# Kernel optimization log

Hardware: AMD Instinct MI355X
Metric: run time of the kernel (lower is better)

## Reference

```python
import jax, jax.numpy as jnp
import numpy as np

EMBED_DIM = 1024
NUM_HEADS = 16
ROTARY_THETA = 10000.0


def _rotate_half(t):
    d = t.shape[-1] // 2
    t1, t2 = t[..., :d], t[..., d:]
    return jnp.concatenate([-t2, t1], axis=-1)


def _rope_cos_sin(seq_len, head_dim, dtype):
    # inv_freq over even indices, standard RoPE
    inv_freq = 1.0 / (ROTARY_THETA ** (jnp.arange(0, head_dim, 2, dtype=jnp.float32) / head_dim))
    freqs = jnp.arange(seq_len, dtype=jnp.float32)[:, None] * inv_freq[None, :]  # (S, D/2)
    emb = jnp.concatenate([freqs, freqs], axis=-1)  # (S, D)
    # broadcast over (b, s, h, d)
    return jnp.cos(emb).astype(dtype)[None, :, None, :], jnp.sin(emb).astype(dtype)[None, :, None, :]


def setup_inputs() -> dict:
    key = jax.random.key(0)
    ks = jax.random.split(key, 4)
    B, S, E = 2, 2048, EMBED_DIM
    scale = 1.0 / np.sqrt(E)
    return {
        "x": jax.random.normal(ks[0], (B, S, E), dtype=jnp.float32),
        "attention_mask": jnp.zeros((B, 1, 1, S), dtype=jnp.float32),
        "Wq": jax.random.normal(ks[1], (E, E), dtype=jnp.float32) * scale,
        "bq": jnp.zeros((E,), dtype=jnp.float32),
        "Wk": jax.random.normal(ks[2], (E, E), dtype=jnp.float32) * scale,
        "bk": jnp.zeros((E,), dtype=jnp.float32),
        "Wv": jax.random.normal(ks[3], (E, E), dtype=jnp.float32) * scale,
        "bv": jnp.zeros((E,), dtype=jnp.float32),
    }


def reference(x, attention_mask, Wq, bq, Wk, bk, Wv, bv):
    B, S, E = x.shape
    H = NUM_HEADS
    D = E // H

    q = (x @ Wq + bq).reshape(B, S, H, D)
    k = (x @ Wk + bk).reshape(B, S, H, D)
    v = (x @ Wv + bv).reshape(B, S, H, D)

    cos, sin = _rope_cos_sin(S, D, q.dtype)
    q = q * cos + _rotate_half(q) * sin
    k = k * cos + _rotate_half(k) * sin

    # attention_mask: additive padding bias (b,1,1,k) broadcast over heads & queries
    scores = jnp.einsum("bqhd,bkhd->bhqk", q, k) / jnp.sqrt(jnp.asarray(D, dtype=q.dtype))
    scores = scores + attention_mask  # broadcasts to (b,h,q,k)
    attn = jax.nn.softmax(scores, axis=-1)
    out = jnp.einsum("bhqk,bkhd->bqhd", attn, v)
    return out.reshape(B, S, E)
```

## Files before the change

### kernel.cpp

```cpp
#include <hip/hip_runtime.h>

typedef __attribute__((ext_vector_type(8)))  short bf16x8;
typedef __attribute__((ext_vector_type(4)))  float f32x4;
typedef __attribute__((ext_vector_type(16))) float f32x16;
typedef __attribute__((ext_vector_type(4)))  unsigned u32x4;
typedef __attribute__((ext_vector_type(4)))  _Float16 f16x4;

#define B_  2
#define S_  2048
#define H_  16
#define D_  64
#define E_  1024
#define M_  (B_*S_)
#define L2E 1.44269504f

__device__ __forceinline__ unsigned short f2bf(float f){
  unsigned x = __builtin_bit_cast(unsigned, f);
  x += 0x7fffu + ((x >> 16) & 1u);
  return (unsigned short)(x >> 16);
}
__device__ __forceinline__ unsigned pk_bf16(float lo, float hi){
  unsigned short a = __builtin_bit_cast(unsigned short, (__bf16)lo);
  unsigned short b = __builtin_bit_cast(unsigned short, (__bf16)hi);
  return (unsigned)a | ((unsigned)b << 16);
}

#define GLD16(gp, lp) __builtin_amdgcn_global_load_lds( \
    (const __attribute__((address_space(1))) unsigned*)(gp), \
    (__attribute__((address_space(3))) unsigned*)(lp), 16, 0, 0)

__global__ __launch_bounds__(256) void k_tables(const float* __restrict__ mask,
                                                float* ct, float* st, float* maskC){
  int i = blockIdx.x*256 + threadIdx.x;
  int s = i >> 5, f = i & 31;
  float invf = powf(10000.0f, -(float)f / 32.0f);
  float ph = (float)s * invf;
  ct[i] = cosf(ph);
  st[i] = sinf(ph);
  if(i < B_*S_) maskC[i] = fmaf(mask[i], L2E, -17.0f);
}

__global__ __launch_bounds__(256) void k_cvt(const float* __restrict__ in, short* __restrict__ out){
  int i = (blockIdx.x*256 + threadIdx.x)*4;
  float4 v = *(const float4*)(in + i);
  typedef __attribute__((ext_vector_type(4))) short s16x4;
  s16x4 o = { (short)f2bf(v.x), (short)f2bf(v.y), (short)f2bf(v.z), (short)f2bf(v.w) };
  *(s16x4*)(out + i) = o;
}

__global__ __launch_bounds__(256) void k_wt(const float* __restrict__ Wq, const float* __restrict__ Wk,
                                            const float* __restrict__ Wv, short* __restrict__ wt){
  const float* W = blockIdx.z==0 ? Wq : (blockIdx.z==1 ? Wk : Wv);
  short* out = wt + (size_t)blockIdx.z*E_*E_;
  __shared__ short tile[64][72];
  int nb = blockIdx.x*64, kb = blockIdx.y*64;
  int t = threadIdx.x;
  {
    int r = t>>2, c0 = (t&3)*16;
    const float* src = W + (size_t)(kb+r)*E_ + nb + c0;
    #pragma unroll
    for(int i=0;i<4;i++){
      float4 v = *(const float4*)(src + i*4);
      tile[r][c0+i*4+0] = (short)f2bf(v.x);
      tile[r][c0+i*4+1] = (short)f2bf(v.y);
      tile[r][c0+i*4+2] = (short)f2bf(v.z);
      tile[r][c0+i*4+3] = (short)f2bf(v.w);
    }
  }
  __syncthreads();
  {
    int n = t>>2, k0 = (t&3)*16;
    short* dst = out + (size_t)(nb+n)*E_ + kb + k0;
    bf16x8 o0, o1;
    #pragma unroll
    for(int i=0;i<8;i++){ o0[i] = tile[k0+i][n]; o1[i] = tile[k0+8+i][n]; }
    *(bf16x8*)dst = o0;
    *(bf16x8*)(dst+8) = o1;
  }
}

__global__ __launch_bounds__(256) void k_gemm(const short* __restrict__ A, const short* __restrict__ WT,
                                              const float* __restrict__ biasq, const float* __restrict__ biask,
                                              const float* __restrict__ biasv,
                                              short* __restrict__ oq, short* __restrict__ ok, short* __restrict__ ov,
                                              const float* __restrict__ cost, const float* __restrict__ sint){
  const int z = blockIdx.z;
  const short* Bw = WT + (size_t)z*E_*E_;
  const float* bias = z==0 ? biasq : (z==1 ? biask : biasv);
  short* out = z==0 ? oq : (z==1 ? ok : ov);
  __shared__ short As[128*32];
  __shared__ short Bs[128*32];
  const int t = threadIdx.x, lane = t & 63, wid = t >> 6;
  const int mb = blockIdx.x*128, nb = blockIdx.y*128;
  const int wm = (wid>>1)*64, wn = (wid&1)*64;
  f32x4 acc[4][4] = {};
  for(int kt=0; kt<E_/32; kt++){
    __syncthreads();
    {
      int f0 = t, f1 = t + 256;
      GLD16(A  + (size_t)(mb + (f0>>2))*E_ + kt*32 + (f0&3)*8, &As[f0*8]);
      GLD16(A  + (size_t)(mb + (f1>>2))*E_ + kt*32 + (f1&3)*8, &As[f1*8]);
      GLD16(Bw + (size_t)(nb + (f0>>2))*E_ + kt*32 + (f0&3)*8, &Bs[f0*8]);
      GLD16(Bw + (size_t)(nb + (f1>>2))*E_ + kt*32 + (f1&3)*8, &Bs[f1*8]);
    }
    __syncthreads();
    bf16x8 af[4], bfv[4];
    #pragma unroll
    for(int mf=0; mf<4; mf++)
      af[mf] = *(const bf16x8*)&As[(wm + mf*16 + (lane&15))*32 + (lane>>4)*8];
    #pragma unroll
    for(int nf=0; nf<4; nf++)
      bfv[nf] = *(const bf16x8*)&Bs[(wn + nf*16 + (lane&15))*32 + (lane>>4)*8];
    #pragma unroll
    for(int mf=0; mf<4; mf++)
      #pragma unroll
      for(int nf=0; nf<4; nf++)
        acc[mf][nf] = __builtin_amdgcn_mfma_f32_16x16x32_bf16(af[mf], bfv[nf], acc[mf][nf], 0, 0, 0);
  }
  const int col16 = lane & 15, rg = lane >> 4;
  float bvs[4];
  #pragma unroll
  for(int nf=0; nf<4; nf++) bvs[nf] = bias[nb + wn + nf*16 + col16];
  if(z == 2){
    #pragma unroll
    for(int mf=0; mf<4; mf++)
      #pragma unroll
      for(int nf=0; nf<4; nf++)
        #pragma unroll
        for(int r=0; r<4; r++){
          int row = mb + wm + mf*16 + rg*4 + r;
          out[(size_t)row*E_ + nb + wn + nf*16 + col16] = (short)f2bf(acc[mf][nf][r] + bvs[nf]);
        }
  } else {
    const float qs = (z==0) ? (0.125f*L2E) : 1.0f;
    #pragma unroll
    for(int mf=0; mf<4; mf++)
      #pragma unroll
      for(int r=0; r<4; r++){
        int row = mb + wm + mf*16 + rg*4 + r;
        int srow = row & (S_-1);
        const float* cb = cost + (size_t)srow*32;
        const float* sb = sint + (size_t)srow*32;
        #pragma unroll
        for(int nf=0; nf<2; nf++){
          int d = nf*16 + col16;
          float c = cb[d], sn = sb[d];
          float x0 = acc[mf][nf][r]   + bvs[nf];
          float x1 = acc[mf][nf+2][r] + bvs[nf+2];
          out[(size_t)row*E_ + nb + wn + nf*16 + col16]     = (short)f2bf((x0*c - x1*sn)*qs);
          out[(size_t)row*E_ + nb + wn + (nf+2)*16 + col16] = (short)f2bf((x1*c + x0*sn)*qs);
        }
      }
  }
}

__global__ __launch_bounds__(256) void k_vt(const short* __restrict__ v, short* __restrict__ vt){
  __shared__ short tl[64][72];
  const int b = blockIdx.z, h = blockIdx.y, s0 = blockIdx.x*64;
  const int t = threadIdx.x;
  {
    int r = t>>2, c0 = (t&3)*16;
    const short* src = v + ((size_t)(b*S_ + s0 + r)*H_ + h)*D_ + c0;
    *(bf16x8*)&tl[r][c0]   = *(const bf16x8*)src;
    *(bf16x8*)&tl[r][c0+8] = *(const bf16x8*)(src+8);
  }
  __syncthreads();
  {
    int d = t>>2, t0 = (t&3)*16;
    short* dst = vt + ((size_t)(b*H_ + h)*D_ + d)*S_ + s0 + t0;
    bf16x8 o0, o1;
    #pragma unroll
    for(int i=0;i<8;i++){ o0[i] = tl[t0+i][d]; o1[i] = tl[t0+8+i][d]; }
    *(bf16x8*)dst = o0;
    *(bf16x8*)(dst+8) = o1;
  }
}

__global__ __launch_bounds__(256,4) void k_attn(
    const short* __restrict__ qg, const short* __restrict__ kg,
    const short* __restrict__ vtg, const float* __restrict__ maskC,
    float* __restrict__ o0g, _Float16* __restrict__ o1g, float* __restrict__ lpart){
  __shared__ short Ks[2][64*72];
  __shared__ short Vs[2][64*72];
  const int b = blockIdx.z, h = blockIdx.y;
  const int qb = blockIdx.x >> 1, sp = blockIdx.x & 1;
  const int tid = threadIdx.x, wid = tid>>6, lane = tid&63;
  const int l31 = lane & 31, hl = lane >> 5;
  const int qw = qb*128 + wid*32;
  const int rr = tid>>3, ch = tid&7;
  const int kb0 = sp*16;
  const int NT = 16;

  bf16x8 qf[4];
  {
    const short* qp = qg + ((size_t)(b*S_ + qw + l31)*H_ + h)*D_;
    #pragma unroll
    for(int dk=0; dk<4; dk++)
      qf[dk] = *(const bf16x8*)(qp + dk*16 + hl*8);
  }
  f32x16 O0 = {}, O1 = {};
  float l_run = 0.f;
  const float* mrow = maskC + (size_t)b*S_;

  bf16x8 ka, kc, va, vc;
#define LOADT(kb) { \
    const short* ks_ = kg + ((size_t)(b*S_ + (kb)*64 + rr)*H_ + h)*D_ + ch*8; \
    ka = *(const bf16x8*)ks_;  kc = *(const bf16x8*)(ks_ + 32*H_*D_); \
    const short* vs_ = vtg + ((size_t)(b*H_ + h)*D_ + rr)*S_ + (kb)*64 + ch*8; \
    va = *(const bf16x8*)vs_;  vc = *(const bf16x8*)(vs_ + 32*S_); }
#define WRITET(pp) { \
    *(bf16x8*)&Ks[pp][rr*72 + ch*8]      = ka; \
    *(bf16x8*)&Ks[pp][(rr+32)*72 + ch*8] = kc; \
    *(bf16x8*)&Vs[pp][rr*72 + ch*8]      = va; \
    *(bf16x8*)&Vs[pp][(rr+32)*72 + ch*8] = vc; }

  LOADT(kb0);
  WRITET(0);
  LOADT(kb0+1);
  __syncthreads();

  int p = 0;
  for(int tt=0; tt<NT; tt++){
    f32x16 s0 = {}, s1 = {};
    #pragma unroll
    for(int dk=0; dk<4; dk++){
      bf16x8 kf0 = *(const bf16x8*)&Ks[p][(l31)*72 + dk*16 + hl*8];
      bf16x8 kf1 = *(const bf16x8*)&Ks[p][(32+l31)*72 + dk*16 + hl*8];
      s0 = __builtin_amdgcn_mfma_f32_32x32x16_bf16(kf0, qf[dk], s0, 0,0,0);
      s1 = __builtin_amdgcn_mfma_f32_32x32x16_bf16(kf1, qf[dk], s1, 0,0,0);
    }
    {
      const float* mt = mrow + (kb0+tt)*64 + hl*4;
      #pragma unroll
      for(int bb=0; bb<4; bb++){
        f32x4 mv0 = *(const f32x4*)(mt + bb*8);
        f32x4 mv1 = *(const f32x4*)(mt + 32 + bb*8);
        #pragma unroll
        for(int a=0; a<4; a++){ s0[bb*4+a] += mv0[a]; s1[bb*4+a] += mv1[a]; }
      }
    }
    #pragma unroll
    for(int i=0;i<16;i++) s0[i] = __builtin_amdgcn_exp2f(s0[i]);
    #pragma unroll
    for(int i=0;i<16;i++) s1[i] = __builtin_amdgcn_exp2f(s1[i]);
    float la=0.f, lb=0.f, lc=0.f, ld=0.f;
    #pragma unroll
    for(int i=0;i<4;i++){
      la += s0[i];   lb += s0[4+i];  lc += s0[8+i];  ld += s0[12+i];
      la += s1[i];   lb += s1[4+i];  lc += s1[8+i];  ld += s1[12+i];
    }
    float ls = (la+lb)+(lc+ld);
    ls += __shfl_xor(ls, 32);
    l_run += ls;

    unsigned w0a[8], w1a[8];
    #pragma unroll
    for(int c=0;c<8;c++){
      int base = (c&3)*4;
      float p0 = (c & 4) ? s1[base+0] : s0[base+0];
      float p1 = (c & 4) ? s1[base+1] : s0[base+1];
      float p2 = (c & 4) ? s1[base+2] : s0[base+2];
      float p3 = (c & 4) ? s1[base+3] : s0[base+3];
      w0a[c] = pk_bf16(p0, p1);
      w1a[c] = pk_bf16(p2, p3);
    }

    if(tt+1 < NT){
      WRITET(p^1);
      if(tt+2 < NT) LOADT(kb0+tt+2);
    }

    #pragma unroll
    for(int ksl=0; ksl<4; ksl++){
      unsigned a0 = w0a[2*ksl], b0 = w0a[2*ksl+1];
      unsigned a1 = w1a[2*ksl], b1 = w1a[2*ksl+1];
      asm("v_permlane32_swap_b32 %0, %1" : "+v"(a0), "+v"(b0));
      asm("v_permlane32_swap_b32 %0, %1" : "+v"(a1), "+v"(b1));
      u32x4 pw = { a0, a1, b0, b1 };
      bf16x8 pf = __builtin_bit_cast(bf16x8, pw);
      bf16x8 vf0 = *(const bf16x8*)&Vs[p][(l31)*72 + ksl*16 + hl*8];
      bf16x8 vf1 = *(const bf16x8*)&Vs[p][(32+l31)*72 + ksl*16 + hl*8];
      O0 = __builtin_amdgcn_mfma_f32_32x32x16_bf16(pf, vf0, O0, 0,0,0);
      O1 = __builtin_amdgcn_mfma_f32_32x32x16_bf16(pf, vf1, O1, 0,0,0);
    }
    __syncthreads();
    p ^= 1;
  }
#undef LOADT
#undef WRITET

  if(sp == 0){
    #pragma unroll
    for(int bb=0; bb<4; bb++)
      #pragma unroll
      for(int a=0; a<4; a++){
        int qrow = qw + a + 8*bb + 4*hl;
        float* op = o0g + ((size_t)(b*S_ + qrow)*H_ + h)*D_;
        op[l31]      = O0[bb*4+a];
        op[32 + l31] = O1[bb*4+a];
      }
  } else {
    #pragma unroll
    for(int bb=0; bb<4; bb++)
      #pragma unroll
      for(int a=0; a<4; a++){
        int qrow = qw + a + 8*bb + 4*hl;
        _Float16* op = o1g + ((size_t)(b*S_ + qrow)*H_ + h)*D_;
        op[l31]      = (_Float16)O0[bb*4+a];
        op[32 + l31] = (_Float16)O1[bb*4+a];
      }
  }
  if(lane < 32)
    lpart[(size_t)sp*(M_*H_) + (size_t)(b*S_ + qw + l31)*H_ + h] = l_run;
}

__global__ __launch_bounds__(256) void k_comb(float* __restrict__ out, const _Float16* __restrict__ o1,
                                              const float* __restrict__ lpart){
  int i = blockIdx.x*256 + threadIdx.x;
  int idx = i*4;
  int lidx = idx >> 6;
  float linv = 1.f / (lpart[lidx] + lpart[M_*H_ + lidx]);
  f32x4 a = *(f32x4*)(out + idx);
  f16x4 bb = *(const f16x4*)(o1 + idx);
  f32x4 r = { (a[0] + (float)bb[0])*linv, (a[1] + (float)bb[1])*linv,
              (a[2] + (float)bb[2])*linv, (a[3] + (float)bb[3])*linv };
  *(f32x4*)(out + idx) = r;
}

extern "C" void kernel_launch(void* const* d_in, const int* in_sizes, int n_in,
                              void* d_out, int out_size, void* d_ws, size_t ws_size,
                              hipStream_t stream){
  (void)in_sizes; (void)n_in; (void)out_size; (void)ws_size;
  const float* x    = (const float*)d_in[0];
  const float* mask = (const float*)d_in[1];
  const float* Wq   = (const float*)d_in[2];
  const float* bq   = (const float*)d_in[3];
  const float* Wk   = (const float*)d_in[4];
  const float* bk   = (const float*)d_in[5];
  const float* Wv   = (const float*)d_in[6];
  const float* bv   = (const float*)d_in[7];
  float* out = (float*)d_out;
  char* ws = (char*)d_ws;
  float* cost  = (float*)(ws);
  float* sint  = (float*)(ws + (256u<<10));
  float* maskC = (float*)(ws + (512u<<10));
  float* lpart = (float*)(ws + (768u<<10));
  short* xb    = (short*)(ws + (2u<<20));
  short* wt    = (short*)(ws + (10u<<20));
  short* qb    = (short*)(ws + (16u<<20));
  short* kb    = (short*)(ws + (24u<<20));
  short* vb    = (short*)(ws + (32u<<20));
  short* vtb   = xb;
  _Float16* o1 = (_Float16*)vb;

  k_tables<<<dim3(256), dim3(256), 0, stream>>>(mask, cost, sint, maskC);
  k_cvt<<<dim3(4096), dim3(256), 0, stream>>>(x, xb);
  k_wt<<<dim3(16,16,3), dim3(256), 0, stream>>>(Wq, Wk, Wv, wt);
  k_gemm<<<dim3(32,8,3), dim3(256), 0, stream>>>(xb, wt, bq, bk, bv, qb, kb, vb, cost, sint);
  k_vt<<<dim3(32,16,2), dim3(256), 0, stream>>>(vb, vtb);
  k_attn<<<dim3(32,16,2), dim3(256), 0, stream>>>(qb, kb, vtb, maskC, out, o1, lpart);
  k_comb<<<dim3(4096), dim3(256), 0, stream>>>(out, o1, lpart);
}
```

Before: 128.0 us.

## Fuse table/cvt kernels, write V transposed from GEMM, remap attention grid, add setprio

Merges the RoPE/mask table kernel into the x-to-bf16 conversion kernel. The V projection epilogue now writes V directly in the transposed (b,h,d,s) layout, so the separate transpose kernel is dropped. The attention grid becomes 1D with a swizzled block-to-(b,h,q) mapping, likely to group blocks that share K/V or to spread them across XCDs. s_setprio is raised around the MFMA sections. Two launches and a V round trip are removed, but the transposed V stores are strided 8-byte writes, which may coalesce poorly.

```diff
diff --git a/kernel.cpp b/kernel.cpp
--- a/kernel.cpp
+++ b/kernel.cpp
@@ -1,6 +1,7 @@
 #include <hip/hip_runtime.h>
 
 typedef __attribute__((ext_vector_type(8)))  short bf16x8;
+typedef __attribute__((ext_vector_type(4)))  short s16x4;
 typedef __attribute__((ext_vector_type(4)))  float f32x4;
 typedef __attribute__((ext_vector_type(16))) float f32x16;
 typedef __attribute__((ext_vector_type(4)))  unsigned u32x4;
@@ -29,23 +30,22 @@
     (const __attribute__((address_space(1))) unsigned*)(gp), \
     (__attribute__((address_space(3))) unsigned*)(lp), 16, 0, 0)
 
-__global__ __launch_bounds__(256) void k_tables(const float* __restrict__ mask,
-                                                float* ct, float* st, float* maskC){
+__global__ __launch_bounds__(256) void k_cvt(const float* __restrict__ in, short* __restrict__ out,
+                                             const float* __restrict__ mask,
+                                             float* ct, float* st, float* maskC){
   int i = blockIdx.x*256 + threadIdx.x;
-  int s = i >> 5, f = i & 31;
-  float invf = powf(10000.0f, -(float)f / 32.0f);
-  float ph = (float)s * invf;
-  ct[i] = cosf(ph);
-  st[i] = sinf(ph);
-  if(i < B_*S_) maskC[i] = fmaf(mask[i], L2E, -17.0f);
-}
-
-__global__ __launch_bounds__(256) void k_cvt(const float* __restrict__ in, short* __restrict__ out){
-  int i = (blockIdx.x*256 + threadIdx.x)*4;
-  float4 v = *(const float4*)(in + i);
-  typedef __attribute__((ext_vector_type(4))) short s16x4;
+  if(i < S_*32){
+    int s = i >> 5, f = i & 31;
+    float invf = powf(10000.0f, -(float)f / 32.0f);
+    float ph = (float)s * invf;
+    ct[i] = cosf(ph);
+    st[i] = sinf(ph);
+    if(i < B_*S_) maskC[i] = fmaf(mask[i], L2E, -17.0f);
+  }
+  int j = i*4;
+  float4 v = *(const float4*)(in + j);
   s16x4 o = { (short)f2bf(v.x), (short)f2bf(v.y), (short)f2bf(v.z), (short)f2bf(v.w) };
-  *(s16x4*)(out + i) = o;
+  *(s16x4*)(out + j) = o;
 }
 
 __global__ __launch_bounds__(256) void k_wt(const float* __restrict__ Wq, const float* __restrict__ Wk,
@@ -82,12 +82,11 @@
 __global__ __launch_bounds__(256) void k_gemm(const short* __restrict__ A, const short* __restrict__ WT,
                                               const float* __restrict__ biasq, const float* __restrict__ biask,
                                               const float* __restrict__ biasv,
-                                              short* __restrict__ oq, short* __restrict__ ok, short* __restrict__ ov,
+                                              short* __restrict__ oq, short* __restrict__ ok, short* __restrict__ ovt,
                                               const float* __restrict__ cost, const float* __restrict__ sint){
   const int z = blockIdx.z;
   const short* Bw = WT + (size_t)z*E_*E_;
   const float* bias = z==0 ? biasq : (z==1 ? biask : biasv);
-  short* out = z==0 ? oq : (z==1 ? ok : ov);
   __shared__ short As[128*32];
   __shared__ short Bs[128*32];
   const int t = threadIdx.x, lane = t & 63, wid = t >> 6;
@@ -123,15 +122,20 @@
   for(int nf=0; nf<4; nf++) bvs[nf] = bias[nb + wn + nf*16 + col16];
   if(z == 2){
     #pragma unroll
-    for(int mf=0; mf<4; mf++)
-      #pragma unroll
-      for(int nf=0; nf<4; nf++)
-        #pragma unroll
-        for(int r=0; r<4; r++){
-          int row = mb + wm + mf*16 + rg*4 + r;
-          out[(size_t)row*E_ + nb + wn + nf*16 + col16] = (short)f2bf(acc[mf][nf][r] + bvs[nf]);
-        }
+    for(int mf=0; mf<4; mf++){
+      int row0 = mb + wm + mf*16 + rg*4;
+      int bb2 = row0 >> 11, ss = row0 & (S_-1);
+      #pragma unroll
+      for(int nf=0; nf<4; nf++){
+        int e = nb + wn + nf*16 + col16;
+        int hh = e >> 6, dd = e & 63;
+        s16x4 w = { (short)f2bf(acc[mf][nf][0]+bvs[nf]), (short)f2bf(acc[mf][nf][1]+bvs[nf]),
+                    (short)f2bf(acc[mf][nf][2]+bvs[nf]), (short)f2bf(acc[mf][nf][3]+bvs[nf]) };
+        *(s16x4*)(ovt + ((size_t)(bb2*H_+hh)*D_+dd)*S_ + ss) = w;
+      }
+    }
   } else {
+    short* out = (z==0) ? oq : ok;
     const float qs = (z==0) ? (0.125f*L2E) : 1.0f;
     #pragma unroll
     for(int mf=0; mf<4; mf++)
@@ -154,36 +158,18 @@
   }
 }
 
-__global__ __launch_bounds__(256) void k_vt(const short* __restrict__ v, short* __restrict__ vt){
-  __shared__ short tl[64][72];
-  const int b = blockIdx.z, h = blockIdx.y, s0 = blockIdx.x*64;
-  const int t = threadIdx.x;
-  {
-    int r = t>>2, c0 = (t&3)*16;
-    const short* src = v + ((size_t)(b*S_ + s0 + r)*H_ + h)*D_ + c0;
-    *(bf16x8*)&tl[r][c0]   = *(const bf16x8*)src;
-    *(bf16x8*)&tl[r][c0+8] = *(const bf16x8*)(src+8);
-  }
-  __syncthreads();
-  {
-    int d = t>>2, t0 = (t&3)*16;
-    short* dst = vt + ((size_t)(b*H_ + h)*D_ + d)*S_ + s0 + t0;
-    bf16x8 o0, o1;
-    #pragma unroll
-    for(int i=0;i<8;i++){ o0[i] = tl[t0+i][d]; o1[i] = tl[t0+8+i][d]; }
-    *(bf16x8*)dst = o0;
-    *(bf16x8*)(dst+8) = o1;
-  }
-}
-
 __global__ __launch_bounds__(256,4) void k_attn(
     const short* __restrict__ qg, const short* __restrict__ kg,
     const short* __restrict__ vtg, const float* __restrict__ maskC,
     float* __restrict__ o0g, _Float16* __restrict__ o1g, float* __restrict__ lpart){
   __shared__ short Ks[2][64*72];
   __shared__ short Vs[2][64*72];
-  const int b = blockIdx.z, h = blockIdx.y;
-  const int qb = blockIdx.x >> 1, sp = blockIdx.x & 1;
+  const int flat = blockIdx.x;
+  const int v = flat >> 3;
+  const int bh = (flat & 7)*4 + (v >> 5);
+  const int inner = v & 31;
+  const int qb = inner >> 1, sp = inner & 1;
+  const int h = bh & 15, b = bh >> 4;
   const int tid = threadIdx.x, wid = tid>>6, lane = tid&63;
   const int l31 = lane & 31, hl = lane >> 5;
   const int qw = qb*128 + wid*32;
@@ -222,6 +208,7 @@
   int p = 0;
   for(int tt=0; tt<NT; tt++){
     f32x16 s0 = {}, s1 = {};
+    __builtin_amdgcn_s_setprio(1);
     #pragma unroll
     for(int dk=0; dk<4; dk++){
       bf16x8 kf0 = *(const bf16x8*)&Ks[p][(l31)*72 + dk*16 + hl*8];
@@ -229,6 +216,7 @@
       s0 = __builtin_amdgcn_mfma_f32_32x32x16_bf16(kf0, qf[dk], s0, 0,0,0);
       s1 = __builtin_amdgcn_mfma_f32_32x32x16_bf16(kf1, qf[dk], s1, 0,0,0);
     }
+    __builtin_amdgcn_s_setprio(0);
     {
       const float* mt = mrow + (kb0+tt)*64 + hl*4;
       #pragma unroll
@@ -270,6 +258,7 @@
       if(tt+2 < NT) LOADT(kb0+tt+2);
     }
 
+    __builtin_amdgcn_s_setprio(1);
     #pragma unroll
     for(int ksl=0; ksl<4; ksl++){
       unsigned a0 = w0a[2*ksl], b0 = w0a[2*ksl+1];
@@ -283,6 +272,7 @@
       O0 = __builtin_amdgcn_mfma_f32_32x32x16_bf16(pf, vf0, O0, 0,0,0);
       O1 = __builtin_amdgcn_mfma_f32_32x32x16_bf16(pf, vf1, O1, 0,0,0);
     }
+    __builtin_amdgcn_s_setprio(0);
     __syncthreads();
     p ^= 1;
   }
@@ -349,15 +339,12 @@
   short* wt    = (short*)(ws + (10u<<20));
   short* qb    = (short*)(ws + (16u<<20));
   short* kb    = (short*)(ws + (24u<<20));
-  short* vb    = (short*)(ws + (32u<<20));
-  short* vtb   = xb;
-  _Float16* o1 = (_Float16*)vb;
-
-  k_tables<<<dim3(256), dim3(256), 0, stream>>>(mask, cost, sint, maskC);
-  k_cvt<<<dim3(4096), dim3(256), 0, stream>>>(x, xb);
+  short* vtb   = (short*)(ws + (32u<<20));
+  _Float16* o1 = (_Float16*)xb;
+
+  k_cvt<<<dim3(4096), dim3(256), 0, stream>>>(x, xb, mask, cost, sint, maskC);
   k_wt<<<dim3(16,16,3), dim3(256), 0, stream>>>(Wq, Wk, Wv, wt);
-  k_gemm<<<dim3(32,8,3), dim3(256), 0, stream>>>(xb, wt, bq, bk, bv, qb, kb, vb, cost, sint);
-  k_vt<<<dim3(32,16,2), dim3(256), 0, stream>>>(vb, vtb);
-  k_attn<<<dim3(32,16,2), dim3(256), 0, stream>>>(qb, kb, vtb, maskC, out, o1, lpart);
+  k_gemm<<<dim3(32,8,3), dim3(256), 0, stream>>>(xb, wt, bq, bk, bv, qb, kb, vtb, cost, sint);
+  k_attn<<<dim3(1024), dim3(256), 0, stream>>>(qb, kb, vtb, maskC, out, o1, lpart);
   k_comb<<<dim3(4096), dim3(256), 0, stream>>>(out, o1, lpart);
 }
```

New measurement: 118.1 us. -7.7%, faster.
